# Optimization experiments

Measured on AMD Instinct MI355X. Metric: run time of the kernel, lower is better.

The kernel has to match this reference:

```python
import jax, jax.numpy as jnp
import numpy as np

D_HIST = 64
LO, HI = -3.0, 3.0
FALL_OFF = 0.02
EPS = 1e-6


def setup_inputs() -> dict:
    key = jax.random.key(0)
    k1, k2 = jax.random.split(key)
    x = jax.random.uniform(k1, (8, 3, 256, 256), dtype=jnp.float32)
    y = jax.random.uniform(k2, (8, 3, 256, 256), dtype=jnp.float32)
    return {"x": x, "y": y}


def _hist_feature(img):
    # img: (B, 3, H, W)
    B = img.shape[0]
    flat = (img + EPS).reshape(B, 3, -1)            # (B, 3, N)
    i_y = jnp.sqrt(jnp.sum(jnp.square(flat), axis=1))  # (B, N) pixel intensity
    lr, lg, lb = jnp.log(flat[:, 0]), jnp.log(flat[:, 1]), jnp.log(flat[:, 2])
    ur = lr - lg
    vr = lr - lb
    ug, vg = -ur, -ur + vr
    ub, vb = -vr, -vr + ur
    centers = jnp.linspace(LO, HI, D_HIST, dtype=img.dtype)  # (D,)

    def rbf(d):
        # inverse-quadratic kernel vs bin centers -> (B, N, D)
        return 1.0 / (1.0 + jnp.square(jnp.abs(d[..., None] - centers) / FALL_OFF))

    def hist_c(uc, vc):
        # weighted outer-product reduction over pixels (the bmm): (B, D, D)
        return jnp.einsum('bn,bnu,bnv->buv', i_y, rbf(uc), rbf(vc))

    hist = jnp.stack([hist_c(ur, vr), hist_c(ug, vg), hist_c(ub, vb)], axis=1)  # (B,3,D,D)
    total = jnp.sum(hist, axis=(1, 2, 3), keepdims=True)
    return hist / total


def reference(x, y):
    x_hist = _hist_feature(x)
    y_hist = _hist_feature(y)
    diff = jnp.sqrt(y_hist) - jnp.sqrt(x_hist)
    h = jnp.sum(jnp.square(diff), axis=(1, 2, 3))  # (B,)
    h_norm = jnp.sqrt(h) * jnp.sqrt(jnp.asarray(0.5, dtype=h.dtype))
    return jnp.mean(h_norm)
```

## Files before the change

### kernel.cpp

```cpp
#include <hip/hip_runtime.h>
#include <math.h>

#define N_PIX 65536
#define EPSF 1e-6f
#define CHUNKS 16
#define PX_PER_CHUNK 4096
#define PX_PER_WAVE 1024
#define N_TILES (PX_PER_WAVE / 64)
#define N_JOBS 48
#define LN2_50 34.65735903f

typedef __attribute__((ext_vector_type(2))) float f2;
using short8 = __attribute__((ext_vector_type(8))) short;
using f32x4  = __attribute__((ext_vector_type(4))) float;

__device__ __forceinline__ float rcp_fast(float x) { return __builtin_amdgcn_rcpf(x); }

#if __has_builtin(__builtin_amdgcn_cvt_pk_bf16_f32)
typedef __attribute__((ext_vector_type(2))) __bf16 bf16x2_t;
__device__ __forceinline__ uint32_t pk_bf16(float a, float b) {
    return __builtin_bit_cast(uint32_t, __builtin_amdgcn_cvt_pk_bf16_f32(a, b));
}
#else
__device__ __forceinline__ uint32_t pk_bf16(float a, float b) {
    const uint32_t ua = __builtin_bit_cast(uint32_t, a) + 0x8000u;
    const uint32_t ub = __builtin_bit_cast(uint32_t, b) + 0x8000u;
    return __builtin_amdgcn_perm(ub, ua, 0x07060302u);
}
#endif

__device__ __forceinline__ float4 phaseA(float pr, float pg, float pb, int c) {
    const float r  = pr + EPSF;
    const float g  = pg + EPSF;
    const float bl = pb + EPSF;
    const float wgt = sqrtf(fmaf(r, r, fmaf(g, g, bl * bl)));
    const float lr = __log2f(r), lg = __log2f(g), lb2 = __log2f(bl);
    const float l0 = (c == 0) ? lr : ((c == 1) ? lg : lb2);
    const float lu = (c == 0) ? lg : lr;
    const float lv = (c == 2) ? lg : lb2;
    return make_float4((l0 - lu) * LN2_50, (l0 - lv) * LN2_50, wgt, 0.0f);
}

__global__ __launch_bounds__(256, 4) void hist_kernel(
    const float* __restrict__ x, const float* __restrict__ y,
    float* __restrict__ partial)
{
    const int blk = blockIdx.x;
    const int chunk = blk & (CHUNKS - 1);
    const int job = blk / CHUNKS;
    const int c = job % 3;
    const int ib = job / 3;
    const int img = ib >> 3;
    const int b = ib & 7;
    const float* __restrict__ src = (img == 0 ? x : y) + (size_t)b * 3 * N_PIX;

    __shared__ __align__(16) float lds[4096];
    const int tid = threadIdx.x;
    const int lane = tid & 63;
    const int wv = tid >> 6;
    float* __restrict__ wbuf = lds + wv * 288;

    const int quad = lane >> 4;
    const int l15 = lane & 15;
    f2 ncb01, ncb23;
    {
        const float c0 = (-3.0f + (float)(l15)      * (6.0f / 63.0f)) * 50.0f;
        const float c1 = (-3.0f + (float)(16 + l15) * (6.0f / 63.0f)) * 50.0f;
        const float c2 = (-3.0f + (float)(32 + l15) * (6.0f / 63.0f)) * 50.0f;
        const float c3 = (-3.0f + (float)(48 + l15) * (6.0f / 63.0f)) * 50.0f;
        ncb01 = (f2){-c0, -c1};
        ncb23 = (f2){-c2, -c3};
    }
    const f2 one2 = {1.0f, 1.0f};

    f32x4 acc[16];
#pragma unroll
    for (int i = 0; i < 16; ++i) acc[i] = (f32x4){0.f, 0.f, 0.f, 0.f};

    const int px0 = chunk * PX_PER_CHUNK + wv * PX_PER_WAVE;

    float pr, pg, pb;
    {
        const int n = px0 + lane;
        pr = src[n]; pg = src[N_PIX + n]; pb = src[2 * N_PIX + n];
    }

#pragma unroll 1
    for (int st = 0; st < N_TILES; ++st) {
        const float4 uvw = phaseA(pr, pg, pb, c);
        *(float4*)(wbuf + lane * 4 + (lane >> 3) * 4) = uvw;

        if (st + 1 < N_TILES) {
            const int n2 = px0 + (st + 1) * 64 + lane;
            pr = src[n2]; pg = src[N_PIX + n2]; pb = src[2 * N_PIX + n2];
        }

#pragma unroll
        for (int h = 0; h < 2; ++h) {
            const int base = h * 32 + quad * 8;
            const float4* __restrict__ pbase =
                (const float4*)(wbuf + base * 4 + (base >> 3) * 4);
            int aU[4][4], aV[4][4];

#pragma unroll
            for (int jp = 0; jp < 4; ++jp) {
                const float4 pe = pbase[2 * jp];
                const float4 po = pbase[2 * jp + 1];

                float aue[4], auo[4], bve[4], bvo[4];
#pragma unroll
                for (int eo = 0; eo < 2; ++eo) {
                    const float ru = eo ? po.x : pe.x;
                    const float rv = eo ? po.y : pe.y;
                    const float rw = eo ? po.z : pe.z;
                    float* au = eo ? auo : aue;
                    float* bv = eo ? bvo : bve;

                    const f2 ruu = {ru, ru};
                    const f2 tu01 = ruu + ncb01;
                    const f2 tu23 = ruu + ncb23;
                    const f2 qu01 = __builtin_elementwise_fma(tu01, tu01, one2);
                    const f2 qu23 = __builtin_elementwise_fma(tu23, tu23, one2);
                    const float pu01 = qu01.x * qu01.y;
                    const float pu23 = qu23.x * qu23.y;
                    const float Ru = rcp_fast(pu01 * pu23) * rw;
                    const float ru01 = Ru * pu23, ru23 = Ru * pu01;
                    au[0] = ru01 * qu01.y; au[1] = ru01 * qu01.x;
                    au[2] = ru23 * qu23.y; au[3] = ru23 * qu23.x;

                    const f2 rvv = {rv, rv};
                    const f2 tv01 = rvv + ncb01;
                    const f2 tv23 = rvv + ncb23;
                    const f2 qv01 = __builtin_elementwise_fma(tv01, tv01, one2);
                    const f2 qv23 = __builtin_elementwise_fma(tv23, tv23, one2);
                    const float pv01 = qv01.x * qv01.y;
                    const float pv23 = qv23.x * qv23.y;
                    const float Rv = rcp_fast(pv01 * pv23);
                    const float rv01 = Rv * pv23, rv23 = Rv * pv01;
                    bv[0] = rv01 * qv01.y; bv[1] = rv01 * qv01.x;
                    bv[2] = rv23 * qv23.y; bv[3] = rv23 * qv23.x;
                }
#pragma unroll
                for (int mt = 0; mt < 4; ++mt) {
                    aU[mt][jp] = pk_bf16(aue[mt], auo[mt]);
                    aV[mt][jp] = pk_bf16(bve[mt], bvo[mt]);
                }
            }

            short8 af[4], bf[4];
#pragma unroll
            for (int mt = 0; mt < 4; ++mt) {
                af[mt] = __builtin_bit_cast(short8,
                    make_int4(aU[mt][0], aU[mt][1], aU[mt][2], aU[mt][3]));
                bf[mt] = __builtin_bit_cast(short8,
                    make_int4(aV[mt][0], aV[mt][1], aV[mt][2], aV[mt][3]));
            }
#pragma unroll
            for (int mt = 0; mt < 4; ++mt)
#pragma unroll
                for (int nt = 0; nt < 4; ++nt)
                    acc[mt * 4 + nt] = __builtin_amdgcn_mfma_f32_16x16x32_bf16(
                        af[mt], bf[nt], acc[mt * 4 + nt], 0, 0, 0);
        }
    }

    float* __restrict__ outp = partial + (size_t)blk * 4096;
#pragma unroll 1
    for (int ch = 0; ch < 4; ++ch) {
        __syncthreads();
#pragma unroll
        for (int nt = 0; nt < 4; ++nt)
            *(f32x4*)(lds + wv * 1024 + nt * 256 + lane * 4) = acc[ch * 4 + nt];
        __syncthreads();
        const int e4 = tid * 4;
        const f32x4 s0 = *(const f32x4*)(lds +        e4);
        const f32x4 s1 = *(const f32x4*)(lds + 1024 + e4);
        const f32x4 s2 = *(const f32x4*)(lds + 2048 + e4);
        const f32x4 s3 = *(const f32x4*)(lds + 3072 + e4);
        const f32x4 s = (s0 + s1) + (s2 + s3);
        const int l = tid & 63;
        const int n = ((tid >> 6) << 4) | (l & 15);
        float* op = outp + (ch * 16 + (l >> 4) * 4) * 64 + n;
        op[0] = s.x; op[64] = s.y; op[128] = s.z; op[192] = s.w;
    }
}

__global__ __launch_bounds__(256) void reduce_partials_kernel(
    const float* __restrict__ partial, float* __restrict__ hist,
    float* __restrict__ totals)
{
    const int job = blockIdx.x >> 4;
    const int e = ((blockIdx.x & 15) << 8) | threadIdx.x;
    const float* p = partial + (size_t)job * CHUNKS * 4096 + e;
    float s = 0.0f;
#pragma unroll
    for (int k = 0; k < CHUNKS; ++k) s += p[(size_t)k * 4096];
    hist[(size_t)job * 4096 + e] = s;

    __shared__ float red[4];
    float v = s;
#pragma unroll
    for (int o = 32; o > 0; o >>= 1) v += __shfl_down(v, o, 64);
    if ((threadIdx.x & 63) == 0) red[threadIdx.x >> 6] = v;
    __syncthreads();
    if (threadIdx.x == 0)
        atomicAdd(&totals[job / 3], red[0] + red[1] + red[2] + red[3]);
}

__global__ __launch_bounds__(1024) void loss_kernel(
    const float* __restrict__ hist, const float* __restrict__ totals,
    float* __restrict__ out)
{
    const int b = blockIdx.x;
    __shared__ float red[16];
    const int tid = threadIdx.x;
    const float* xh = hist + (size_t)(b * 3) * 4096;
    const float* yh = hist + (size_t)((8 + b) * 3) * 4096;
    const float invx = 1.0f / totals[b];
    const float invy = 1.0f / totals[8 + b];

    float h = 0.0f;
    for (int i = tid; i < 3 * 4096; i += 1024) {
        const float d = sqrtf(yh[i] * invy) - sqrtf(xh[i] * invx);
        h = fmaf(d, d, h);
    }
#pragma unroll
    for (int o = 32; o > 0; o >>= 1) h += __shfl_down(h, o, 64);
    if ((tid & 63) == 0) red[tid >> 6] = h;
    __syncthreads();
    if (tid == 0) {
        float hs = 0.0f;
#pragma unroll
        for (int i = 0; i < 16; ++i) hs += red[i];
        atomicAdd(out, sqrtf(0.5f * hs) * 0.125f);
    }
}

extern "C" void kernel_launch(void* const* d_in, const int* in_sizes, int n_in,
                              void* d_out, int out_size, void* d_ws, size_t ws_size,
                              hipStream_t stream)
{
    const float* x = (const float*)d_in[0];
    const float* y = (const float*)d_in[1];
    float* ws = (float*)d_ws;
    float* partial = ws;
    float* hist = ws + (size_t)N_JOBS * CHUNKS * 4096;
    float* totals = hist + (size_t)N_JOBS * 4096;
    float* outf = (float*)d_out;

    hipMemsetAsync(totals, 0, 16 * sizeof(float), stream);
    hipMemsetAsync(outf, 0, sizeof(float), stream);
    hipLaunchKernelGGL(hist_kernel, dim3(N_JOBS * CHUNKS), dim3(256), 0, stream,
                       x, y, partial);
    hipLaunchKernelGGL(reduce_partials_kernel, dim3(N_JOBS * 16), dim3(256), 0, stream,
                       partial, hist, totals);
    hipLaunchKernelGGL(loss_kernel, dim3(8), dim3(1024), 0, stream, hist, totals, outf);
}
```

Baseline: 175.0 us.

## Fuse partial reduction, totals and loss into one finalize kernel

Replaces the partial-reduction kernel, the loss kernel and both memsets with a single 8-block finalize kernel that sums the chunk partials, computes per-image totals and the Hellinger loss in registers. The output zeroing moves into the histogram kernel. This removes launches, memsets and the intermediate hist/totals round trip, but the whole partial buffer is now reduced by only 8 blocks, which limits memory parallelism.

```diff
diff --git a/kernel.cpp b/kernel.cpp
--- a/kernel.cpp
+++ b/kernel.cpp
@@ -43,7 +43,7 @@
 
 __global__ __launch_bounds__(256, 4) void hist_kernel(
     const float* __restrict__ x, const float* __restrict__ y,
-    float* __restrict__ partial)
+    float* __restrict__ partial, float* __restrict__ out)
 {
     const int blk = blockIdx.x;
     const int chunk = blk & (CHUNKS - 1);
@@ -53,6 +53,8 @@
     const int img = ib >> 3;
     const int b = ib & 7;
     const float* __restrict__ src = (img == 0 ? x : y) + (size_t)b * 3 * N_PIX;
+
+    if (blk == 0 && threadIdx.x == 0) out[0] = 0.0f;
 
     __shared__ __align__(16) float lds[4096];
     const int tid = threadIdx.x;
@@ -185,53 +187,63 @@
     }
 }
 
-__global__ __launch_bounds__(256) void reduce_partials_kernel(
-    const float* __restrict__ partial, float* __restrict__ hist,
-    float* __restrict__ totals)
-{
-    const int job = blockIdx.x >> 4;
-    const int e = ((blockIdx.x & 15) << 8) | threadIdx.x;
-    const float* p = partial + (size_t)job * CHUNKS * 4096 + e;
-    float s = 0.0f;
-#pragma unroll
-    for (int k = 0; k < CHUNKS; ++k) s += p[(size_t)k * 4096];
-    hist[(size_t)job * 4096 + e] = s;
-
-    __shared__ float red[4];
-    float v = s;
-#pragma unroll
-    for (int o = 32; o > 0; o >>= 1) v += __shfl_down(v, o, 64);
-    if ((threadIdx.x & 63) == 0) red[threadIdx.x >> 6] = v;
-    __syncthreads();
-    if (threadIdx.x == 0)
-        atomicAdd(&totals[job / 3], red[0] + red[1] + red[2] + red[3]);
-}
-
-__global__ __launch_bounds__(1024) void loss_kernel(
-    const float* __restrict__ hist, const float* __restrict__ totals,
-    float* __restrict__ out)
+__global__ __launch_bounds__(1024) void finalize_kernel(
+    const float* __restrict__ partial, float* __restrict__ out)
 {
     const int b = blockIdx.x;
-    __shared__ float red[16];
     const int tid = threadIdx.x;
-    const float* xh = hist + (size_t)(b * 3) * 4096;
-    const float* yh = hist + (size_t)((8 + b) * 3) * 4096;
-    const float invx = 1.0f / totals[b];
-    const float invy = 1.0f / totals[8 + b];
+    const int wv = tid >> 6;
+    __shared__ float redx[16], redy[16];
+
+    const float* __restrict__ px = partial + (size_t)(b * 3) * CHUNKS * 4096;
+    const float* __restrict__ py = partial + (size_t)((8 + b) * 3) * CHUNKS * 4096;
+
+    float hx[12], hy[12];
+    float tx = 0.0f, ty = 0.0f;
+#pragma unroll
+    for (int i = 0; i < 12; ++i) {
+        const int e = tid + i * 1024;
+        const int c = e >> 12;
+        const int el = e & 4095;
+        const float* __restrict__ bx = px + (size_t)c * CHUNKS * 4096 + el;
+        const float* __restrict__ by = py + (size_t)c * CHUNKS * 4096 + el;
+        float sx = 0.0f, sy = 0.0f;
+#pragma unroll
+        for (int k = 0; k < CHUNKS; ++k) {
+            sx += bx[(size_t)k * 4096];
+            sy += by[(size_t)k * 4096];
+        }
+        hx[i] = sx; hy[i] = sy;
+        tx += sx; ty += sy;
+    }
+
+#pragma unroll
+    for (int o = 32; o > 0; o >>= 1) {
+        tx += __shfl_down(tx, o, 64);
+        ty += __shfl_down(ty, o, 64);
+    }
+    if ((tid & 63) == 0) { redx[wv] = tx; redy[wv] = ty; }
+    __syncthreads();
+    float TX = 0.0f, TY = 0.0f;
+#pragma unroll
+    for (int i = 0; i < 16; ++i) { TX += redx[i]; TY += redy[i]; }
+    const float invx = 1.0f / TX, invy = 1.0f / TY;
 
     float h = 0.0f;
-    for (int i = tid; i < 3 * 4096; i += 1024) {
-        const float d = sqrtf(yh[i] * invy) - sqrtf(xh[i] * invx);
+#pragma unroll
+    for (int i = 0; i < 12; ++i) {
+        const float d = sqrtf(hy[i] * invy) - sqrtf(hx[i] * invx);
         h = fmaf(d, d, h);
     }
 #pragma unroll
     for (int o = 32; o > 0; o >>= 1) h += __shfl_down(h, o, 64);
-    if ((tid & 63) == 0) red[tid >> 6] = h;
+    __syncthreads();
+    if ((tid & 63) == 0) redx[wv] = h;
     __syncthreads();
     if (tid == 0) {
         float hs = 0.0f;
 #pragma unroll
-        for (int i = 0; i < 16; ++i) hs += red[i];
+        for (int i = 0; i < 16; ++i) hs += redx[i];
         atomicAdd(out, sqrtf(0.5f * hs) * 0.125f);
     }
 }
@@ -242,17 +254,11 @@
 {
     const float* x = (const float*)d_in[0];
     const float* y = (const float*)d_in[1];
-    float* ws = (float*)d_ws;
-    float* partial = ws;
-    float* hist = ws + (size_t)N_JOBS * CHUNKS * 4096;
-    float* totals = hist + (size_t)N_JOBS * 4096;
+    float* partial = (float*)d_ws;
     float* outf = (float*)d_out;
 
-    hipMemsetAsync(totals, 0, 16 * sizeof(float), stream);
-    hipMemsetAsync(outf, 0, sizeof(float), stream);
     hipLaunchKernelGGL(hist_kernel, dim3(N_JOBS * CHUNKS), dim3(256), 0, stream,
-                       x, y, partial);
-    hipLaunchKernelGGL(reduce_partials_kernel, dim3(N_JOBS * 16), dim3(256), 0, stream,
-                       partial, hist, totals);
-    hipLaunchKernelGGL(loss_kernel, dim3(8), dim3(1024), 0, stream, hist, totals, outf);
-}
+                       x, y, partial, outf);
+    hipLaunchKernelGGL(finalize_kernel, dim3(8), dim3(1024), 0, stream,
+                       partial, outf);
+}
```

Measured after the change: 250.3 us. 43.0% more time.

## Fuse partial reduction and loss via Bhattacharyya cross-sum identity

Applied to the files above, without the earlier changes.

Rewrites the loss algebraically: the Hellinger distance sum of squared sqrt differences equals 2 - 2*sum(sqrt(x*y))/sqrt(Sx*Sy), so the reduce kernel sums x and y partials together and accumulates Sx, Sy and the cross term with atomics. This removes the intermediate histogram write, the separate loss kernel and both memsets; the accumulator is zeroed inside the first kernel instead. The identity form 1-rho can suffer cancellation when histograms are nearly equal, which is handled only by clamping at zero.

```diff
diff --git a/kernel.cpp b/kernel.cpp
--- a/kernel.cpp
+++ b/kernel.cpp
@@ -8,6 +8,7 @@
 #define PX_PER_WAVE 1024
 #define N_TILES (PX_PER_WAVE / 64)
 #define N_JOBS 48
+#define N_BLOCKS (N_JOBS * CHUNKS)
 #define LN2_50 34.65735903f
 
 typedef __attribute__((ext_vector_type(2))) float f2;
@@ -43,7 +44,7 @@
 
 __global__ __launch_bounds__(256, 4) void hist_kernel(
     const float* __restrict__ x, const float* __restrict__ y,
-    float* __restrict__ partial)
+    float* __restrict__ partial, float* __restrict__ accum)
 {
     const int blk = blockIdx.x;
     const int chunk = blk & (CHUNKS - 1);
@@ -54,8 +55,10 @@
     const int b = ib & 7;
     const float* __restrict__ src = (img == 0 ? x : y) + (size_t)b * 3 * N_PIX;
 
+    const int tid = threadIdx.x;
+    if (blk == 0 && tid < 24) accum[tid] = 0.0f;
+
     __shared__ __align__(16) float lds[4096];
-    const int tid = threadIdx.x;
     const int lane = tid & 63;
     const int wv = tid >> 6;
     float* __restrict__ wbuf = lds + wv * 288;
@@ -185,54 +188,52 @@
     }
 }
 
-__global__ __launch_bounds__(256) void reduce_partials_kernel(
-    const float* __restrict__ partial, float* __restrict__ hist,
-    float* __restrict__ totals)
-{
-    const int job = blockIdx.x >> 4;
+__global__ __launch_bounds__(256) void reduce_cross_kernel(
+    const float* __restrict__ partial, float* __restrict__ accum)
+{
+    const int jx = blockIdx.x >> 4;
+    const int bb = jx / 3;
     const int e = ((blockIdx.x & 15) << 8) | threadIdx.x;
-    const float* p = partial + (size_t)job * CHUNKS * 4096 + e;
-    float s = 0.0f;
-#pragma unroll
-    for (int k = 0; k < CHUNKS; ++k) s += p[(size_t)k * 4096];
-    hist[(size_t)job * 4096 + e] = s;
-
-    __shared__ float red[4];
-    float v = s;
-#pragma unroll
-    for (int o = 32; o > 0; o >>= 1) v += __shfl_down(v, o, 64);
-    if ((threadIdx.x & 63) == 0) red[threadIdx.x >> 6] = v;
+    const float* px = partial + (size_t)jx * CHUNKS * 4096 + e;
+    const float* py = partial + (size_t)(24 + jx) * CHUNKS * 4096 + e;
+
+    float sx = 0.0f, sy = 0.0f;
+#pragma unroll
+    for (int k = 0; k < CHUNKS; ++k) {
+        sx += px[(size_t)k * 4096];
+        sy += py[(size_t)k * 4096];
+    }
+    float cr = sqrtf(sx * sy);
+
+#pragma unroll
+    for (int o = 32; o > 0; o >>= 1) {
+        sx += __shfl_down(sx, o, 64);
+        sy += __shfl_down(sy, o, 64);
+        cr += __shfl_down(cr, o, 64);
+    }
+    __shared__ float red[12];
+    const int wv = threadIdx.x >> 6;
+    if ((threadIdx.x & 63) == 0) {
+        red[wv] = sx; red[4 + wv] = sy; red[8 + wv] = cr;
+    }
     __syncthreads();
-    if (threadIdx.x == 0)
-        atomicAdd(&totals[job / 3], red[0] + red[1] + red[2] + red[3]);
-}
-
-__global__ __launch_bounds__(1024) void loss_kernel(
-    const float* __restrict__ hist, const float* __restrict__ totals,
-    float* __restrict__ out)
-{
-    const int b = blockIdx.x;
-    __shared__ float red[16];
-    const int tid = threadIdx.x;
-    const float* xh = hist + (size_t)(b * 3) * 4096;
-    const float* yh = hist + (size_t)((8 + b) * 3) * 4096;
-    const float invx = 1.0f / totals[b];
-    const float invy = 1.0f / totals[8 + b];
-
-    float h = 0.0f;
-    for (int i = tid; i < 3 * 4096; i += 1024) {
-        const float d = sqrtf(yh[i] * invy) - sqrtf(xh[i] * invx);
-        h = fmaf(d, d, h);
-    }
-#pragma unroll
-    for (int o = 32; o > 0; o >>= 1) h += __shfl_down(h, o, 64);
-    if ((tid & 63) == 0) red[tid >> 6] = h;
-    __syncthreads();
-    if (tid == 0) {
-        float hs = 0.0f;
-#pragma unroll
-        for (int i = 0; i < 16; ++i) hs += red[i];
-        atomicAdd(out, sqrtf(0.5f * hs) * 0.125f);
+    if (threadIdx.x == 0) {
+        atomicAdd(&accum[bb],      red[0] + red[1] + red[2] + red[3]);
+        atomicAdd(&accum[8 + bb],  red[4] + red[5] + red[6] + red[7]);
+        atomicAdd(&accum[16 + bb], red[8] + red[9] + red[10] + red[11]);
+    }
+}
+
+__global__ void final_kernel(const float* __restrict__ accum, float* __restrict__ out)
+{
+    if (threadIdx.x == 0) {
+        float s = 0.0f;
+#pragma unroll
+        for (int b = 0; b < 8; ++b) {
+            const float rho = accum[16 + b] * __builtin_amdgcn_rsqf(accum[b] * accum[8 + b]);
+            s += sqrtf(fmaxf(1.0f - rho, 0.0f));
+        }
+        out[0] = s * 0.125f;
     }
 }
 
@@ -244,15 +245,12 @@
     const float* y = (const float*)d_in[1];
     float* ws = (float*)d_ws;
     float* partial = ws;
-    float* hist = ws + (size_t)N_JOBS * CHUNKS * 4096;
-    float* totals = hist + (size_t)N_JOBS * 4096;
+    float* accum = ws + (size_t)N_BLOCKS * 4096;
     float* outf = (float*)d_out;
 
-    hipMemsetAsync(totals, 0, 16 * sizeof(float), stream);
-    hipMemsetAsync(outf, 0, sizeof(float), stream);
-    hipLaunchKernelGGL(hist_kernel, dim3(N_JOBS * CHUNKS), dim3(256), 0, stream,
-                       x, y, partial);
-    hipLaunchKernelGGL(reduce_partials_kernel, dim3(N_JOBS * 16), dim3(256), 0, stream,
-                       partial, hist, totals);
-    hipLaunchKernelGGL(loss_kernel, dim3(8), dim3(1024), 0, stream, hist, totals, outf);
-}
+    hipLaunchKernelGGL(hist_kernel, dim3(N_BLOCKS), dim3(256), 0, stream,
+                       x, y, partial, accum);
+    hipLaunchKernelGGL(reduce_cross_kernel, dim3(24 * 16), dim3(256), 0, stream,
+                       partial, accum);
+    hipLaunchKernelGGL(final_kernel, dim3(1), dim3(64), 0, stream, accum, outf);
+}
```

Measured after the change: 167.2 us. 4.4% less time.
